# Kernel tuning notes

Hardware: AMD Instinct MI355X
Metric: run time of the kernel (lower is better)

## Reference

```python
import jax, jax.numpy as jnp
import numpy as np

N_GENES = 2000
D_MODEL = 256
N_LAYERS = 4
D_STATE = 16
D_CONV = 4
EXPAND = 2
D_INNER = EXPAND * D_MODEL  # 512
DT_RANK = (D_MODEL + 15) // 16  # 16


def layer_norm(x, w, b, eps=1e-5):
    mu = jnp.mean(x, axis=-1, keepdims=True)
    var = jnp.mean((x - mu) ** 2, axis=-1, keepdims=True)
    return (x - mu) * jax.lax.rsqrt(var + eps) * w + b


def mamba_mixer(h, in_w, cw, cb, xp_w, dtp_w, dtp_b, A_log, Dvec, out_w):
    # h: [B, L, d_model]
    B, L, _ = h.shape
    xz = jnp.einsum('bld,ed->ble', h, in_w)            # [B,L,2*Di]
    u, z = jnp.split(xz, 2, axis=-1)                    # [B,L,Di] each
    # causal depthwise conv1d (kernel D_CONV)
    up = jnp.pad(u, ((0, 0), (D_CONV - 1, 0), (0, 0)))
    u = sum(up[:, k:k + L, :] * cw[:, k] for k in range(D_CONV)) + cb
    u = jax.nn.silu(u)
    # input-dependent dt, B, C
    xdbc = jnp.einsum('bld,ed->ble', u, xp_w)           # [B,L,dt_rank+2N]
    dt_r = xdbc[..., :DT_RANK]
    Bm = xdbc[..., DT_RANK:DT_RANK + D_STATE]           # [B,L,N]
    Cm = xdbc[..., DT_RANK + D_STATE:]                  # [B,L,N]
    dt = jax.nn.softplus(jnp.einsum('blr,dr->bld', dt_r, dtp_w) + dtp_b)  # [B,L,Di]
    A = -jnp.exp(A_log)                                 # [Di,N]
    dA = jnp.exp(dt[..., None] * A)                     # [B,L,Di,N]
    dBu = dt[..., None] * Bm[:, :, None, :] * u[..., None]

    def step(hst, inp):
        a, bu = inp
        hst = a * hst + bu
        return hst, hst

    h0 = jnp.zeros((B, D_INNER, D_STATE), dA.dtype)
    _, hs = jax.lax.scan(step, h0, (jnp.moveaxis(dA, 1, 0), jnp.moveaxis(dBu, 1, 0)))
    y = jnp.einsum('lbdn,lbn->bld', hs, jnp.moveaxis(Cm, 1, 0)) + u * Dvec
    y = y * jax.nn.silu(z)
    return jnp.einsum('bld,ed->ble', y, out_w)          # [B,L,d_model]


def setup_inputs() -> dict:
    key = jax.random.key(0)
    ks = jax.random.split(key, 16)
    nl = N_LAYERS
    inp = {
        'x': jax.random.normal(ks[0], (2, N_GENES), jnp.float32),
        'bulk_in_w': jax.random.normal(ks[1], (D_MODEL,), jnp.float32),
        'bulk_in_b': jnp.zeros((D_MODEL,), jnp.float32),
        'gene_emb': jax.random.normal(ks[2], (1, N_GENES, D_MODEL), jnp.float32) * 0.02,
        'mod_emb': jax.random.normal(ks[3], (1, 1, D_MODEL), jnp.float32) * 0.02,
        'ln_w': jnp.ones((nl, D_MODEL), jnp.float32),
        'ln_b': jnp.zeros((nl, D_MODEL), jnp.float32),
        'in_proj_w': jax.random.normal(ks[4], (nl, 2 * D_INNER, D_MODEL), jnp.float32) * (D_MODEL ** -0.5),
        'conv_w': jax.random.normal(ks[5], (nl, D_INNER, D_CONV), jnp.float32) * (D_CONV ** -0.5),
        'conv_b': jnp.zeros((nl, D_INNER), jnp.float32),
        'x_proj_w': jax.random.normal(ks[6], (nl, DT_RANK + 2 * D_STATE, D_INNER), jnp.float32) * (D_INNER ** -0.5),
        'dt_proj_w': jax.random.normal(ks[7], (nl, D_INNER, DT_RANK), jnp.float32) * 0.01,
        'dt_proj_b': jnp.full((nl, D_INNER), -4.0, jnp.float32),
        'A_log': jnp.broadcast_to(jnp.log(jnp.arange(1, D_STATE + 1, dtype=jnp.float32)), (nl, D_INNER, D_STATE)).copy(),
        'D': jnp.ones((nl, D_INNER), jnp.float32),
        'out_proj_w': jax.random.normal(ks[8], (nl, D_MODEL, D_INNER), jnp.float32) * (D_INNER ** -0.5),
        'fin_w': jnp.ones((D_MODEL,), jnp.float32),
        'fin_b': jnp.zeros((D_MODEL,), jnp.float32),
        'head_w': jax.random.normal(ks[9], (D_MODEL,), jnp.float32) * (D_MODEL ** -0.5),
        'head_b': jnp.zeros((), jnp.float32),
    }
    return inp


def reference(x, bulk_in_w, bulk_in_b, gene_emb, mod_emb, ln_w, ln_b, in_proj_w,
              conv_w, conv_b, x_proj_w, dt_proj_w, dt_proj_b, A_log, D, out_proj_w,
              fin_w, fin_b, head_w, head_b):
    # token embed (modality='bulk'); Linear(1,d_model) == x[...,None]*w + b
    h = x[..., None] * bulk_in_w + bulk_in_b + gene_emb + mod_emb  # [B,L,d_model]
    for i in range(N_LAYERS):
        h = h + mamba_mixer(layer_norm(h, ln_w[i], ln_b[i]), in_proj_w[i], conv_w[i],
                            conv_b[i], x_proj_w[i], dt_proj_w[i], dt_proj_b[i],
                            A_log[i], D[i], out_proj_w[i])
    h = layer_norm(h, fin_w, fin_b)
    y = jnp.einsum('bld,d->bl', h, head_w) + head_b  # bulk head, squeeze(-1)
    return y
```

## Files before the change

### kernel.cpp

```cpp
#include <hip/hip_runtime.h>
#include <math.h>

#define B_  2
#define L_  2000
#define DM_ 256
#define DI_ 512
#define DS_ 16
#define NL_ 4
#define BL_ (B_*L_)
#define BLP_ 4096
#define NC_ 125
#define CL_ 16
#define NST_ (B_*DI_*DS_)

typedef unsigned short ushort_t;
typedef __attribute__((ext_vector_type(8))) short bf16x8;
typedef __attribute__((ext_vector_type(4))) float f32x4;

__device__ __forceinline__ float siluf(float x) {
    return x / (1.f + __expf(-x));
}

__device__ __forceinline__ ushort_t f2bf(float x) {
    unsigned int u = __float_as_uint(x);
    unsigned int r = (u + 0x7FFFu + ((u >> 16) & 1u)) >> 16;
    return (ushort_t)r;
}

__device__ __forceinline__ float bf2f(ushort_t v) {
    return __uint_as_float(((unsigned int)v) << 16);
}

__global__ __launch_bounds__(256) void embed_f2bf_kernel(
    const float* __restrict__ x, const float* __restrict__ biw,
    const float* __restrict__ bib, const float* __restrict__ ge,
    const float* __restrict__ me, float* __restrict__ h,
    float2* __restrict__ stats,
    const float* __restrict__ s0, const float* __restrict__ s1,
    const float* __restrict__ s2, ushort_t* __restrict__ d0,
    ushort_t* __restrict__ d1, ushort_t* __restrict__ d2,
    int N0, int N1, int N2)
{
    if (blockIdx.x < BL_) {
        __shared__ float sm[8];
        int bl = blockIdx.x, d = threadIdx.x;
        int l = bl % L_;
        float v = x[bl]*biw[d] + bib[d] + ge[(size_t)l*DM_ + d] + me[d];
        h[(size_t)bl*DM_ + d] = v;
        float s = v, q = v*v;
        #pragma unroll
        for (int o = 32; o > 0; o >>= 1) {
            s += __shfl_down(s, o);
            q += __shfl_down(q, o);
        }
        if ((d & 63) == 0) { sm[d >> 6] = s; sm[4 + (d >> 6)] = q; }
        __syncthreads();
        if (d == 0) {
            stats[bl] = make_float2(sm[0]+sm[1]+sm[2]+sm[3], sm[4]+sm[5]+sm[6]+sm[7]);
            stats[BLP_ + bl]   = make_float2(0.f, 0.f);
            stats[2*BLP_ + bl] = make_float2(0.f, 0.f);
            stats[3*BLP_ + bl] = make_float2(0.f, 0.f);
        }
    } else {
        int i = (blockIdx.x - BL_)*256 + threadIdx.x;
        const float* s; ushort_t* d; int j;
        if (i < N0)           { s = s0; d = d0; j = i; }
        else if (i < N0+N1)   { s = s1; d = d1; j = i - N0; }
        else if (i < N0+N1+N2){ s = s2; d = d2; j = i - N0 - N1; }
        else return;
        float4 v = *(const float4*)(s + 4*j);
        ushort_t o[4] = {f2bf(v.x), f2bf(v.y), f2bf(v.z), f2bf(v.w)};
        *(ushort2*)(d + 4*j)     = *(ushort2*)&o[0];
        *(ushort2*)(d + 4*j + 2) = *(ushort2*)&o[2];
    }
}

__global__ __launch_bounds__(256) void gemm_ln_mfma(
    const float* __restrict__ H, const float2* __restrict__ stats,
    const float* __restrict__ lnw, const float* __restrict__ lnb,
    const ushort_t* __restrict__ W, ushort_t* __restrict__ C, int ldc)
{
    __shared__ ushort_t a_s[128*64];
    __shared__ ushort_t b_s[128*64];
    const int r0 = blockIdx.x*128, c0 = blockIdx.y*128;
    const int tid = threadIdx.x;
    const int lane = tid & 63, w = tid >> 6;
    const int wm = (w & 1)*64, wn = (w >> 1)*64;
    const int qd = lane >> 4, l16 = lane & 15;
    f32x4 acc[4][4] = {};
    for (int kc = 0; kc < DM_; kc += 64) {
        #pragma unroll
        for (int q = 0; q < 4; q++) {
            int ch = tid + 256*q;
            int row = ch >> 3, col8 = (ch & 7)*8;
            int grow = r0 + row;
            float2 t0 = stats[grow], t1 = stats[BLP_ + grow];
            float2 t2 = stats[2*BLP_ + grow], t3 = stats[3*BLP_ + grow];
            float sum = t0.x + t1.x + t2.x + t3.x;
            float ssq = t0.y + t1.y + t2.y + t3.y;
            float mu  = sum * (1.f/DM_);
            float inv = rsqrtf(fmaxf(ssq*(1.f/DM_) - mu*mu, 0.f) + 1e-5f);
            const float* hp = H + (size_t)grow*DM_ + kc + col8;
            float4 h0 = *(const float4*)hp, h1 = *(const float4*)(hp + 4);
            const float* wp = lnw + kc + col8;
            const float* bp = lnb + kc + col8;
            float4 w0 = *(const float4*)wp, w1 = *(const float4*)(wp + 4);
            float4 b0 = *(const float4*)bp, b1 = *(const float4*)(bp + 4);
            __align__(16) ushort_t o[8];
            o[0] = f2bf((h0.x - mu)*inv*w0.x + b0.x);
            o[1] = f2bf((h0.y - mu)*inv*w0.y + b0.y);
            o[2] = f2bf((h0.z - mu)*inv*w0.z + b0.z);
            o[3] = f2bf((h0.w - mu)*inv*w0.w + b0.w);
            o[4] = f2bf((h1.x - mu)*inv*w1.x + b1.x);
            o[5] = f2bf((h1.y - mu)*inv*w1.y + b1.y);
            o[6] = f2bf((h1.z - mu)*inv*w1.z + b1.z);
            o[7] = f2bf((h1.w - mu)*inv*w1.w + b1.w);
            *(uint4*)&a_s[row*64 + col8] = *(const uint4*)o;
            *(bf16x8*)&b_s[row*64 + col8] =
                *(const bf16x8*)(W + (size_t)(c0 + row)*DM_ + kc + col8);
        }
        __syncthreads();
        #pragma unroll
        for (int ks = 0; ks < 2; ks++) {
            bf16x8 af[4], bf[4];
            #pragma unroll
            for (int i = 0; i < 4; i++)
                af[i] = *(const bf16x8*)&a_s[(wm + i*16 + l16)*64 + ks*32 + qd*8];
            #pragma unroll
            for (int j = 0; j < 4; j++)
                bf[j] = *(const bf16x8*)&b_s[(wn + j*16 + l16)*64 + ks*32 + qd*8];
            #pragma unroll
            for (int i = 0; i < 4; i++) {
                #pragma unroll
                for (int j = 0; j < 4; j++)
                    acc[i][j] = __builtin_amdgcn_mfma_f32_16x16x32_bf16(
                        af[i], bf[j], acc[i][j], 0, 0, 0);
            }
        }
        __syncthreads();
    }
    #pragma unroll
    for (int i = 0; i < 4; i++) {
        #pragma unroll
        for (int j = 0; j < 4; j++) {
            #pragma unroll
            for (int r = 0; r < 4; r++) {
                int row = r0 + wm + i*16 + qd*4 + r;
                int col = c0 + wn + j*16 + l16;
                C[(size_t)row*ldc + col] = f2bf(acc[i][j][r]);
            }
        }
    }
}

__global__ __launch_bounds__(256) void conv_xproj_kernel(
    const ushort_t* __restrict__ xz, const float* __restrict__ cw,
    const float* __restrict__ cb, const ushort_t* __restrict__ XWb,
    const float* __restrict__ DTW, const float* __restrict__ DTB,
    const float* __restrict__ Alog,
    ushort_t* __restrict__ u_bf, float* __restrict__ bn,
    float* __restrict__ cn, ushort_t* __restrict__ dtn,
    float2* __restrict__ sa)
{
    __shared__ ushort_t xs[19][520];
    __shared__ ushort_t us[16][520];
    __shared__ float ps[4*16*48];
    __shared__ float dtr_s[16][16];
    const int c = blockIdx.x, b = blockIdx.y;
    const int l0 = c * 16;
    const int tid = threadIdx.x;
    const int lane = tid & 63, w = tid >> 6;
    const int qd = lane >> 4, l16 = lane & 15;
    for (int f = tid; f < 19*64; f += 256) {
        int row = f >> 6, c8 = (f & 63)*8;
        int l = l0 - 3 + row;
        uint4 v = {0u, 0u, 0u, 0u};
        if (l >= 0)
            v = *(const uint4*)(xz + (size_t)(b*L_ + l)*1024 + c8);
        *(uint4*)&xs[row][c8] = v;
    }
    __syncthreads();
    #pragma unroll
    for (int q = 0; q < 2; q++) {
        int ch = tid + q*256;
        float4 wv = *(const float4*)(cw + ch*4);
        float bias = cb[ch];
        float x0 = bf2f(xs[0][ch]);
        float x1 = bf2f(xs[1][ch]);
        float x2 = bf2f(xs[2][ch]);
        #pragma unroll
        for (int j = 0; j < 16; j++) {
            float x3 = bf2f(xs[3 + j][ch]);
            float v = fmaf(x0, wv.x, fmaf(x1, wv.y, fmaf(x2, wv.z, fmaf(x3, wv.w, bias))));
            us[j][ch] = f2bf(siluf(v));
            x0 = x1; x1 = x2; x2 = x3;
        }
    }
    __syncthreads();
    for (int f = tid; f < 16*64; f += 256) {
        int row = f >> 6, c8 = (f & 63)*8;
        *(uint4*)(u_bf + (size_t)(b*L_ + l0 + row)*512 + c8) =
            *(const uint4*)&us[row][c8];
    }
    f32x4 acc[3] = {};
    #pragma unroll
    for (int step = 0; step < 4; step++) {
        int k = w*128 + step*32 + qd*8;
        bf16x8 af = *(const bf16x8*)&us[l16][k];
        #pragma unroll
        for (int j = 0; j < 3; j++) {
            bf16x8 bf = *(const bf16x8*)(XWb + (size_t)(j*16 + l16)*512 + k);
            acc[j] = __builtin_amdgcn_mfma_f32_16x16x32_bf16(af, bf, acc[j], 0, 0, 0);
        }
    }
    #pragma unroll
    for (int j = 0; j < 3; j++) {
        #pragma unroll
        for (int r = 0; r < 4; r++)
            ps[(w*16 + qd*4 + r)*48 + j*16 + l16] = acc[j][r];
    }
    __syncthreads();
    #pragma unroll
    for (int e = tid; e < 768; e += 256)
        ps[e] = ps[e] + ps[768 + e] + ps[1536 + e] + ps[2304 + e];
    __syncthreads();
    {
        int row = tid >> 4, n = tid & 15;
        dtr_s[row][n] = ps[row*48 + n];
        size_t base = ((size_t)(b*L_) + l0 + row)*DS_ + n;
        bn[base] = ps[row*48 + 16 + n];
        cn[base] = ps[row*48 + 32 + n];
    }
    __syncthreads();
    #pragma unroll
    for (int q = 0; q < 2; q++) {
        int d = tid + q*256;
        float wreg[16];
        const float4* wp = (const float4*)(DTW + (size_t)d*16);
        #pragma unroll
        for (int k4 = 0; k4 < 4; k4++) {
            float4 v = wp[k4];
            wreg[4*k4+0] = v.x; wreg[4*k4+1] = v.y;
            wreg[4*k4+2] = v.z; wreg[4*k4+3] = v.w;
        }
        float bias = DTB[d];
        float dtv[16];
        #pragma unroll
        for (int r = 0; r < 16; r++) {
            float a = bias;
            #pragma unroll
            for (int k = 0; k < 16; k++) a = fmaf(dtr_s[r][k], wreg[k], a);
            float dt = a > 20.f ? a : log1pf(__expf(a));
            ushort_t dtb16 = f2bf(dt);
            dtn[((size_t)(b*L_) + l0 + r)*DI_ + d] = dtb16;
            dtv[r] = bf2f(dtb16);
        }
        float Ac[DS_], s[DS_], ap[DS_];
        const float* ar = Alog + (size_t)d*DS_;
        #pragma unroll
        for (int n = 0; n < DS_; n++) { Ac[n] = -__expf(ar[n]); s[n] = 0.f; ap[n] = 1.f; }
        #pragma unroll
        for (int l = 0; l < 16; l++) {
            float dt = dtv[l];
            float u  = bf2f(us[l][d]);
            float dtu = dt*u;
            #pragma unroll
            for (int n = 0; n < DS_; n++) {
                float e = __expf(dt*Ac[n]);
                s[n] = fmaf(e, s[n], dtu*ps[l*48 + 16 + n]);
                ap[n] *= e;
            }
        }
        size_t ib = (((size_t)c*B_ + b)*DI_ + d)*DS_;
        float2* sap = sa + ib;
        #pragma unroll
        for (int k = 0; k < 8; k++) {
            float4 t = make_float4(s[2*k], ap[2*k], s[2*k+1], ap[2*k+1]);
            *(float4*)&sap[2*k] = t;
        }
    }
}

__global__ __launch_bounds__(64) void scan_phase2(
    const float2* __restrict__ sa, float* __restrict__ sinc)
{
    const int t = blockIdx.x*64 + threadIdx.x;
    float s = 0.f;
    for (int g = 0; g < 5; g++) {
        float2 v[25];
        #pragma unroll
        for (int i = 0; i < 25; i++)
            v[i] = sa[(size_t)(g*25 + i)*NST_ + t];
        #pragma unroll
        for (int i = 0; i < 25; i++) {
            sinc[(size_t)(g*25 + i)*NST_ + t] = s;
            s = fmaf(v[i].y, s, v[i].x);
        }
    }
}

template<int LAST>
__global__ __launch_bounds__(512) void phase3_fused(
    const ushort_t* __restrict__ dtn, const ushort_t* __restrict__ u_bf,
    const float* __restrict__ bn, const float* __restrict__ cn,
    const float* __restrict__ Alog, const float* __restrict__ Dv,
    const float* __restrict__ sinc, const ushort_t* __restrict__ xz,
    const ushort_t* __restrict__ opw, float* __restrict__ h,
    const float* __restrict__ lnw, const float* __restrict__ lnb,
    const ushort_t* __restrict__ ipw, ushort_t* __restrict__ xz_out,
    const float* __restrict__ hw, const float* __restrict__ hb,
    float* __restrict__ out)
{
    __shared__ float b_sh[CL_*DS_];
    __shared__ float c_sh[CL_*DS_];
    __shared__ ushort_t ys[16][520];
    __shared__ ushort_t a_sh[16][264];
    __shared__ float2 red2[8*16];
    __shared__ float2 muv[16];
    const int c = blockIdx.x, b = blockIdx.y;
    const int l0 = c*CL_;
    const int tid = threadIdx.x;
    const int w = tid >> 6, lane = tid & 63;
    const int qd = lane >> 4, l16 = lane & 15;
    {
        int f = tid & 255;
        size_t src = ((size_t)(b*L_) + l0)*DS_ + f;
        if (tid < 256) b_sh[f] = bn[src];
        else           c_sh[f] = cn[src];
    }
    const int d = tid;
    float Ac[DS_], s[DS_];
    {
        const float* ar = Alog + (size_t)d*DS_;
        #pragma unroll
        for (int n = 0; n < DS_; n++) Ac[n] = -__expf(ar[n]);
        size_t base = (((size_t)c*B_ + b)*DI_ + d)*DS_;
        #pragma unroll
        for (int n4 = 0; n4 < 4; n4++)
            *(float4*)&s[4*n4] = *(const float4*)(sinc + base + 4*n4);
    }
    const float Dd = Dv[d];
    __syncthreads();
    const ushort_t* dtp = dtn  + ((size_t)(b*L_ + l0))*DI_ + d;
    const ushort_t* up  = u_bf + ((size_t)(b*L_ + l0))*DI_ + d;
    const ushort_t* zp  = xz   + ((size_t)(b*L_ + l0))*1024 + 512 + d;
    for (int l = 0; l < CL_; l++) {
        float dt = bf2f(dtp[(size_t)l*DI_]);
        float u  = bf2f(up[(size_t)l*DI_]);
        float z  = bf2f(zp[(size_t)l*1024]);
        float dtu = dt*u;
        float y = u*Dd;
        #pragma unroll
        for (int n = 0; n < DS_; n++) {
            float e = __expf(dt*Ac[n]);
            s[n] = fmaf(e, s[n], dtu*b_sh[l*DS_ + n]);
            y = fmaf(s[n], c_sh[l*DS_ + n], y);
        }
        ys[l][d] = f2bf(y * siluf(z));
    }
    __syncthreads();
    f32x4 acc[2] = {};
    #pragma unroll
    for (int ks = 0; ks < 16; ks++) {
        bf16x8 af = *(const bf16x8*)&ys[l16][ks*32 + qd*8];
        #pragma unroll
        for (int j = 0; j < 2; j++) {
            bf16x8 bfv = *(const bf16x8*)(opw + (size_t)(w*32 + j*16 + l16)*DI_ + ks*32 + qd*8);
            acc[j] = __builtin_amdgcn_mfma_f32_16x16x32_bf16(af, bfv, acc[j], 0, 0, 0);
        }
    }
    float v[2][4];
    #pragma unroll
    for (int r = 0; r < 4; r++) {
        int lrow = qd*4 + r;
        size_t gr = (size_t)(b*L_ + l0 + lrow);
        float sm = 0.f, sq = 0.f;
        #pragma unroll
        for (int j = 0; j < 2; j++) {
            int col = w*32 + j*16 + l16;
            size_t idx = gr*DM_ + col;
            float vv = h[idx] + acc[j][r];
            if (!LAST) h[idx] = vv;
            v[j][r] = vv;
            sm += vv; sq += vv*vv;
        }
        sm += __shfl_xor(sm, 1); sq += __shfl_xor(sq, 1);
        sm += __shfl_xor(sm, 2); sq += __shfl_xor(sq, 2);
        sm += __shfl_xor(sm, 4); sq += __shfl_xor(sq, 4);
        sm += __shfl_xor(sm, 8); sq += __shfl_xor(sq, 8);
        if (l16 == 0) red2[w*16 + lrow] = make_float2(sm, sq);
    }
    __syncthreads();
    if (tid < 16) {
        float sm = 0.f, sq = 0.f;
        #pragma unroll
        for (int ww = 0; ww < 8; ww++) {
            float2 t = red2[ww*16 + tid];
            sm += t.x; sq += t.y;
        }
        float mu  = sm*(1.f/DM_);
        float inv = rsqrtf(fmaxf(sq*(1.f/DM_) - mu*mu, 0.f) + 1e-5f);
        muv[tid] = make_float2(mu, inv);
    }
    __syncthreads();
    if (!LAST) {
        #pragma unroll
        for (int r = 0; r < 4; r++) {
            int lrow = qd*4 + r;
            float2 mi = muv[lrow];
            #pragma unroll
            for (int j = 0; j < 2; j++) {
                int col = w*32 + j*16 + l16;
                a_sh[lrow][col] = f2bf((v[j][r] - mi.x)*mi.y*lnw[col] + lnb[col]);
            }
        }
        __syncthreads();
        f32x4 acc2[8] = {};
        const int n0 = w*128;
        #pragma unroll
        for (int ks = 0; ks < 8; ks++) {
            bf16x8 af = *(const bf16x8*)&a_sh[l16][ks*32 + qd*8];
            #pragma unroll
            for (int j2 = 0; j2 < 8; j2++) {
                bf16x8 bfv = *(const bf16x8*)(ipw + (size_t)(n0 + j2*16 + l16)*DM_ + ks*32 + qd*8);
                acc2[j2] = __builtin_amdgcn_mfma_f32_16x16x32_bf16(af, bfv, acc2[j2], 0, 0, 0);
            }
        }
        #pragma unroll
        for (int j2 = 0; j2 < 8; j2++) {
            #pragma unroll
            for (int r = 0; r < 4; r++) {
                size_t row = (size_t)(b*L_ + l0 + qd*4 + r);
                xz_out[row*1024 + n0 + j2*16 + l16] = f2bf(acc2[j2][r]);
            }
        }
    } else {
        float hd[4];
        #pragma unroll
        for (int r = 0; r < 4; r++) {
            int lrow = qd*4 + r;
            float2 mi = muv[lrow];
            float a = 0.f;
            #pragma unroll
            for (int j = 0; j < 2; j++) {
                int col = w*32 + j*16 + l16;
                float nv = (v[j][r] - mi.x)*mi.y*lnw[col] + lnb[col];
                a = fmaf(nv, hw[col], a);
            }
            hd[r] = a;
        }
        #pragma unroll
        for (int r = 0; r < 4; r++) {
            float x = hd[r];
            x += __shfl_xor(x, 1); x += __shfl_xor(x, 2);
            x += __shfl_xor(x, 4); x += __shfl_xor(x, 8);
            if (l16 == 0) red2[w*16 + qd*4 + r].x = x;
        }
        __syncthreads();
        if (tid < 16) {
            float x = 0.f;
            #pragma unroll
            for (int ww = 0; ww < 8; ww++) x += red2[ww*16 + tid].x;
            out[(size_t)(b*L_) + l0 + tid] = x + hb[0];
        }
    }
}

extern "C" void kernel_launch(void* const* d_in, const int* in_sizes, int n_in,
                              void* d_out, int out_size, void* d_ws, size_t ws_size,
                              hipStream_t stream)
{
    const float* x    = (const float*)d_in[0];
    const float* biw  = (const float*)d_in[1];
    const float* bib  = (const float*)d_in[2];
    const float* ge   = (const float*)d_in[3];
    const float* me   = (const float*)d_in[4];
    const float* lnw  = (const float*)d_in[5];
    const float* lnb  = (const float*)d_in[6];
    const float* ipw  = (const float*)d_in[7];
    const float* cw   = (const float*)d_in[8];
    const float* cb   = (const float*)d_in[9];
    const float* xpw  = (const float*)d_in[10];
    const float* dtw  = (const float*)d_in[11];
    const float* dtb  = (const float*)d_in[12];
    const float* alog = (const float*)d_in[13];
    const float* Dv   = (const float*)d_in[14];
    const float* opw  = (const float*)d_in[15];
    const float* fw   = (const float*)d_in[16];
    const float* fb   = (const float*)d_in[17];
    const float* hw   = (const float*)d_in[18];
    const float* hb   = (const float*)d_in[19];
    float* out = (float*)d_out;

    float* ws  = (float*)d_ws;
    float* h      = ws;
    float2* stats = (float2*)(h + (size_t)BLP_*DM_);
    float* bn     = (float*)(stats + 4*BLP_);
    float* cn     = bn + (size_t)B_*L_*DS_;
    float2* sa    = (float2*)(cn + (size_t)B_*L_*DS_);
    float* sinc   = (float*)(sa + (size_t)NC_*NST_);
    ushort_t* xz_bf = (ushort_t*)(sinc + (size_t)NC_*NST_);
    ushort_t* u_bf  = xz_bf + (size_t)BLP_*1024;
    ushort_t* dtn   = u_bf + (size_t)BLP_*DI_;
    ushort_t* ipwb  = dtn + (size_t)B_*L_*DI_;
    ushort_t* opwb  = ipwb + (size_t)NL_*1024*DM_;
    ushort_t* xpwb  = opwb + (size_t)NL_*DM_*DI_;

    const int N0 = NL_*1024*DM_/4, N1 = NL_*DM_*DI_/4, N2 = NL_*48*512/4;
    const int conv_blocks = (N0+N1+N2 + 255)/256;
    embed_f2bf_kernel<<<BL_ + conv_blocks, 256, 0, stream>>>(
        x, biw, bib, ge, me, h, stats,
        ipw, opw, xpw, ipwb, opwb, xpwb, N0, N1, N2);

    gemm_ln_mfma<<<dim3(BLP_/128, 1024/128), 256, 0, stream>>>(
        h, stats, lnw, lnb, ipwb, xz_bf, 1024);

    for (int i = 0; i < NL_; i++) {
        conv_xproj_kernel<<<dim3(NC_, B_), 256, 0, stream>>>(
            xz_bf, cw + i*DI_*4, cb + i*DI_, xpwb + (size_t)i*48*512,
            dtw + (size_t)i*DI_*16, dtb + i*DI_, alog + (size_t)i*DI_*DS_,
            u_bf, bn, cn, dtn, sa);
        scan_phase2<<<NST_/64, 64, 0, stream>>>(sa, sinc);
        if (i < NL_-1) {
            phase3_fused<0><<<dim3(NC_, B_), 512, 0, stream>>>(
                dtn, u_bf, bn, cn, alog + (size_t)i*DI_*DS_, Dv + i*DI_,
                sinc, xz_bf, opwb + (size_t)i*DM_*DI_, h,
                lnw + (i+1)*DM_, lnb + (i+1)*DM_,
                ipwb + (size_t)(i+1)*1024*DM_, xz_bf,
                nullptr, nullptr, nullptr);
        } else {
            phase3_fused<1><<<dim3(NC_, B_), 512, 0, stream>>>(
                dtn, u_bf, bn, cn, alog + (size_t)i*DI_*DS_, Dv + i*DI_,
                sinc, xz_bf, opwb + (size_t)i*DM_*DI_, h,
                fw, fb,
                nullptr, xz_bf,
                hw, hb, out);
        }
    }
}
```

Before: 414.3 us.

## Fuse phase3 output with next layer's conv/xproj via cooperative launch and halo flags

```diff
diff --git a/kernel.cpp b/kernel.cpp
--- a/kernel.cpp
+++ b/kernel.cpp
@@ -9,26 +9,147 @@
 #define NL_ 4
 #define BL_ (B_*L_)
 #define BLP_ 4096
-#define NC_ 125
-#define CL_ 16
+#define NC_  125
+#define CL_  16
 #define NST_ (B_*DI_*DS_)
 
 typedef unsigned short ushort_t;
 typedef __attribute__((ext_vector_type(8))) short bf16x8;
 typedef __attribute__((ext_vector_type(4))) float f32x4;
 
-__device__ __forceinline__ float siluf(float x) {
-    return x / (1.f + __expf(-x));
-}
-
+__device__ __forceinline__ float siluf(float x) { return x / (1.f + __expf(-x)); }
 __device__ __forceinline__ ushort_t f2bf(float x) {
     unsigned int u = __float_as_uint(x);
-    unsigned int r = (u + 0x7FFFu + ((u >> 16) & 1u)) >> 16;
-    return (ushort_t)r;
-}
-
+    return (ushort_t)((u + 0x7FFFu + ((u >> 16) & 1u)) >> 16);
+}
 __device__ __forceinline__ float bf2f(ushort_t v) {
     return __uint_as_float(((unsigned int)v) << 16);
+}
+
+struct PPart {
+    float b_sh[CL_*DS_];
+    float c_sh[CL_*DS_];
+    ushort_t ys[16][520];
+    ushort_t a_sh[16][264];
+    float2 red2[128];
+    float2 muv[16];
+};
+struct CPart {
+    ushort_t xs[19][520];
+    ushort_t us[16][520];
+    float ps[8*768];
+    float dtr[16][16];
+};
+union SharedF { PPart p; CPart c; };
+
+__device__ __forceinline__ void conv_tail(
+    CPart* S, int tid, int b, int l0, int c,
+    const float* __restrict__ cw, const float* __restrict__ cb,
+    const ushort_t* __restrict__ XWb,
+    const float* __restrict__ DTW, const float* __restrict__ DTB,
+    const float* __restrict__ Alog,
+    ushort_t* __restrict__ u_bf, float* __restrict__ bn,
+    float* __restrict__ cn, ushort_t* __restrict__ dtn,
+    float2* __restrict__ sa)
+{
+    const int lane = tid & 63, w = tid >> 6;
+    const int qd = lane >> 4, l16 = lane & 15;
+    {
+        int ch = tid;
+        float4 wv = *(const float4*)(cw + ch*4);
+        float bias = cb[ch];
+        float x0 = bf2f(S->xs[0][ch]);
+        float x1 = bf2f(S->xs[1][ch]);
+        float x2 = bf2f(S->xs[2][ch]);
+        #pragma unroll
+        for (int j = 0; j < 16; j++) {
+            float x3 = bf2f(S->xs[3 + j][ch]);
+            float v = fmaf(x0, wv.x, fmaf(x1, wv.y, fmaf(x2, wv.z, fmaf(x3, wv.w, bias))));
+            S->us[j][ch] = f2bf(siluf(v));
+            x0 = x1; x1 = x2; x2 = x3;
+        }
+    }
+    __syncthreads();
+    for (int f = tid; f < 16*64; f += 512) {
+        int row = f >> 6, c8 = (f & 63)*8;
+        *(uint4*)(u_bf + (size_t)(b*L_ + l0 + row)*512 + c8) =
+            *(const uint4*)&S->us[row][c8];
+    }
+    f32x4 acc[3] = {};
+    #pragma unroll
+    for (int st = 0; st < 2; st++) {
+        int k = w*64 + st*32 + qd*8;
+        bf16x8 af = *(const bf16x8*)&S->us[l16][k];
+        #pragma unroll
+        for (int j = 0; j < 3; j++) {
+            bf16x8 bv = *(const bf16x8*)(XWb + (size_t)(j*16 + l16)*512 + k);
+            acc[j] = __builtin_amdgcn_mfma_f32_16x16x32_bf16(af, bv, acc[j], 0, 0, 0);
+        }
+    }
+    #pragma unroll
+    for (int j = 0; j < 3; j++)
+        #pragma unroll
+        for (int r = 0; r < 4; r++)
+            S->ps[w*768 + (qd*4 + r)*48 + j*16 + l16] = acc[j][r];
+    __syncthreads();
+    for (int e = tid; e < 768; e += 512) {
+        float v = S->ps[e] + S->ps[768+e] + S->ps[1536+e] + S->ps[2304+e]
+                + S->ps[3072+e] + S->ps[3840+e] + S->ps[4608+e] + S->ps[5376+e];
+        S->ps[e] = v;
+    }
+    __syncthreads();
+    if (tid < 256) {
+        int row = tid >> 4, n = tid & 15;
+        S->dtr[row][n] = S->ps[row*48 + n];
+        size_t base = ((size_t)(b*L_) + l0 + row)*DS_ + n;
+        bn[base] = S->ps[row*48 + 16 + n];
+        cn[base] = S->ps[row*48 + 32 + n];
+    }
+    __syncthreads();
+    {
+        const int d = tid;
+        float wreg[16];
+        const float4* wp = (const float4*)(DTW + (size_t)d*16);
+        #pragma unroll
+        for (int k4 = 0; k4 < 4; k4++) {
+            float4 v = wp[k4];
+            wreg[4*k4+0] = v.x; wreg[4*k4+1] = v.y;
+            wreg[4*k4+2] = v.z; wreg[4*k4+3] = v.w;
+        }
+        float bias = DTB[d];
+        float dtv[16];
+        #pragma unroll
+        for (int r = 0; r < 16; r++) {
+            float a = bias;
+            #pragma unroll
+            for (int k = 0; k < 16; k++) a = fmaf(S->dtr[r][k], wreg[k], a);
+            float dt = a > 20.f ? a : log1pf(__expf(a));
+            ushort_t dtb16 = f2bf(dt);
+            dtn[((size_t)(b*L_) + l0 + r)*DI_ + d] = dtb16;
+            dtv[r] = bf2f(dtb16);
+        }
+        float Ac[DS_], s[DS_], ap[DS_];
+        const float* ar = Alog + (size_t)d*DS_;
+        #pragma unroll
+        for (int n = 0; n < DS_; n++) { Ac[n] = -__expf(ar[n]); s[n] = 0.f; ap[n] = 1.f; }
+        #pragma unroll
+        for (int l = 0; l < 16; l++) {
+            float dt = dtv[l];
+            float u  = bf2f(S->us[l][d]);
+            float dtu = dt*u;
+            #pragma unroll
+            for (int n = 0; n < DS_; n++) {
+                float e = __expf(dt*Ac[n]);
+                s[n] = fmaf(e, s[n], dtu*S->ps[l*48 + 16 + n]);
+                ap[n] *= e;
+            }
+        }
+        size_t ib = (((size_t)c*B_ + b)*DI_ + d)*DS_;
+        float2* sap = sa + ib;
+        #pragma unroll
+        for (int k = 0; k < 8; k++)
+            *(float4*)&sap[2*k] = make_float4(s[2*k], ap[2*k], s[2*k+1], ap[2*k+1]);
+    }
 }
 
 __global__ __launch_bounds__(256) void embed_f2bf_kernel(
@@ -39,7 +160,7 @@
     const float* __restrict__ s0, const float* __restrict__ s1,
     const float* __restrict__ s2, ushort_t* __restrict__ d0,
     ushort_t* __restrict__ d1, ushort_t* __restrict__ d2,
-    int N0, int N1, int N2)
+    int N0, int N1, int N2, unsigned int* __restrict__ flag)
 {
     if (blockIdx.x < BL_) {
         __shared__ float sm[8];
@@ -55,13 +176,12 @@
         }
         if ((d & 63) == 0) { sm[d >> 6] = s; sm[4 + (d >> 6)] = q; }
         __syncthreads();
-        if (d == 0) {
+        if (d == 0)
             stats[bl] = make_float2(sm[0]+sm[1]+sm[2]+sm[3], sm[4]+sm[5]+sm[6]+sm[7]);
-            stats[BLP_ + bl]   = make_float2(0.f, 0.f);
-            stats[2*BLP_ + bl] = make_float2(0.f, 0.f);
-            stats[3*BLP_ + bl] = make_float2(0.f, 0.f);
-        }
     } else {
+        if (blockIdx.x == BL_ && threadIdx.x < 2*NC_)
+            __hip_atomic_store(&flag[threadIdx.x], 0u,
+                               __ATOMIC_RELAXED, __HIP_MEMORY_SCOPE_AGENT);
         int i = (blockIdx.x - BL_)*256 + threadIdx.x;
         const float* s; ushort_t* d; int j;
         if (i < N0)           { s = s0; d = d0; j = i; }
@@ -78,7 +198,7 @@
 __global__ __launch_bounds__(256) void gemm_ln_mfma(
     const float* __restrict__ H, const float2* __restrict__ stats,
     const float* __restrict__ lnw, const float* __restrict__ lnb,
-    const ushort_t* __restrict__ W, ushort_t* __restrict__ C, int ldc)
+    const ushort_t* __restrict__ W, ushort_t* __restrict__ C)
 {
     __shared__ ushort_t a_s[128*64];
     __shared__ ushort_t b_s[128*64];
@@ -94,12 +214,9 @@
             int ch = tid + 256*q;
             int row = ch >> 3, col8 = (ch & 7)*8;
             int grow = r0 + row;
-            float2 t0 = stats[grow], t1 = stats[BLP_ + grow];
-            float2 t2 = stats[2*BLP_ + grow], t3 = stats[3*BLP_ + grow];
-            float sum = t0.x + t1.x + t2.x + t3.x;
-            float ssq = t0.y + t1.y + t2.y + t3.y;
-            float mu  = sum * (1.f/DM_);
-            float inv = rsqrtf(fmaxf(ssq*(1.f/DM_) - mu*mu, 0.f) + 1e-5f);
+            float2 t0 = stats[grow];
+            float mu  = t0.x * (1.f/DM_);
+            float inv = rsqrtf(fmaxf(t0.y*(1.f/DM_) - mu*mu, 0.f) + 1e-5f);
             const float* hp = H + (size_t)grow*DM_ + kc + col8;
             float4 h0 = *(const float4*)hp, h1 = *(const float4*)(hp + 4);
             const float* wp = lnw + kc + col8;
@@ -147,13 +264,13 @@
             for (int r = 0; r < 4; r++) {
                 int row = r0 + wm + i*16 + qd*4 + r;
                 int col = c0 + wn + j*16 + l16;
-                C[(size_t)row*ldc + col] = f2bf(acc[i][j][r]);
+                C[(size_t)row*1024 + col] = f2bf(acc[i][j][r]);
             }
         }
     }
 }
 
-__global__ __launch_bounds__(256) void conv_xproj_kernel(
+__global__ __launch_bounds__(512) void conv0_kernel(
     const ushort_t* __restrict__ xz, const float* __restrict__ cw,
     const float* __restrict__ cb, const ushort_t* __restrict__ XWb,
     const float* __restrict__ DTW, const float* __restrict__ DTB,
@@ -162,123 +279,19 @@
     float* __restrict__ cn, ushort_t* __restrict__ dtn,
     float2* __restrict__ sa)
 {
-    __shared__ ushort_t xs[19][520];
-    __shared__ ushort_t us[16][520];
-    __shared__ float ps[4*16*48];
-    __shared__ float dtr_s[16][16];
-    const int c = blockIdx.x, b = blockIdx.y;
-    const int l0 = c * 16;
+    __shared__ CPart S;
+    const int c = blockIdx.x, b = blockIdx.y, l0 = c*CL_;
     const int tid = threadIdx.x;
-    const int lane = tid & 63, w = tid >> 6;
-    const int qd = lane >> 4, l16 = lane & 15;
-    for (int f = tid; f < 19*64; f += 256) {
+    for (int f = tid; f < 19*64; f += 512) {
         int row = f >> 6, c8 = (f & 63)*8;
         int l = l0 - 3 + row;
-        uint4 v = {0u, 0u, 0u, 0u};
-        if (l >= 0)
-            v = *(const uint4*)(xz + (size_t)(b*L_ + l)*1024 + c8);
-        *(uint4*)&xs[row][c8] = v;
-    }
-    __syncthreads();
-    #pragma unroll
-    for (int q = 0; q < 2; q++) {
-        int ch = tid + q*256;
-        float4 wv = *(const float4*)(cw + ch*4);
-        float bias = cb[ch];
-        float x0 = bf2f(xs[0][ch]);
-        float x1 = bf2f(xs[1][ch]);
-        float x2 = bf2f(xs[2][ch]);
-        #pragma unroll
-        for (int j = 0; j < 16; j++) {
-            float x3 = bf2f(xs[3 + j][ch]);
-            float v = fmaf(x0, wv.x, fmaf(x1, wv.y, fmaf(x2, wv.z, fmaf(x3, wv.w, bias))));
-            us[j][ch] = f2bf(siluf(v));
-            x0 = x1; x1 = x2; x2 = x3;
-        }
-    }
-    __syncthreads();
-    for (int f = tid; f < 16*64; f += 256) {
-        int row = f >> 6, c8 = (f & 63)*8;
-        *(uint4*)(u_bf + (size_t)(b*L_ + l0 + row)*512 + c8) =
-            *(const uint4*)&us[row][c8];
-    }
-    f32x4 acc[3] = {};
-    #pragma unroll
-    for (int step = 0; step < 4; step++) {
-        int k = w*128 + step*32 + qd*8;
-        bf16x8 af = *(const bf16x8*)&us[l16][k];
-        #pragma unroll
-        for (int j = 0; j < 3; j++) {
-            bf16x8 bf = *(const bf16x8*)(XWb + (size_t)(j*16 + l16)*512 + k);
-            acc[j] = __builtin_amdgcn_mfma_f32_16x16x32_bf16(af, bf, acc[j], 0, 0, 0);
-        }
-    }
-    #pragma unroll
-    for (int j = 0; j < 3; j++) {
-        #pragma unroll
-        for (int r = 0; r < 4; r++)
-            ps[(w*16 + qd*4 + r)*48 + j*16 + l16] = acc[j][r];
-    }
-    __syncthreads();
-    #pragma unroll
-    for (int e = tid; e < 768; e += 256)
-        ps[e] = ps[e] + ps[768 + e] + ps[1536 + e] + ps[2304 + e];
-    __syncthreads();
-    {
-        int row = tid >> 4, n = tid & 15;
-        dtr_s[row][n] = ps[row*48 + n];
-        size_t base = ((size_t)(b*L_) + l0 + row)*DS_ + n;
-        bn[base] = ps[row*48 + 16 + n];
-        cn[base] = ps[row*48 + 32 + n];
-    }
-    __syncthreads();
-    #pragma unroll
-    for (int q = 0; q < 2; q++) {
-        int d = tid + q*256;
-        float wreg[16];
-        const float4* wp = (const float4*)(DTW + (size_t)d*16);
-        #pragma unroll
-        for (int k4 = 0; k4 < 4; k4++) {
-            float4 v = wp[k4];
-            wreg[4*k4+0] = v.x; wreg[4*k4+1] = v.y;
-            wreg[4*k4+2] = v.z; wreg[4*k4+3] = v.w;
-        }
-        float bias = DTB[d];
-        float dtv[16];
-        #pragma unroll
-        for (int r = 0; r < 16; r++) {
-            float a = bias;
-            #pragma unroll
-            for (int k = 0; k < 16; k++) a = fmaf(dtr_s[r][k], wreg[k], a);
-            float dt = a > 20.f ? a : log1pf(__expf(a));
-            ushort_t dtb16 = f2bf(dt);
-            dtn[((size_t)(b*L_) + l0 + r)*DI_ + d] = dtb16;
-            dtv[r] = bf2f(dtb16);
-        }
-        float Ac[DS_], s[DS_], ap[DS_];
-        const float* ar = Alog + (size_t)d*DS_;
-        #pragma unroll
-        for (int n = 0; n < DS_; n++) { Ac[n] = -__expf(ar[n]); s[n] = 0.f; ap[n] = 1.f; }
-        #pragma unroll
-        for (int l = 0; l < 16; l++) {
-            float dt = dtv[l];
-            float u  = bf2f(us[l][d]);
-            float dtu = dt*u;
-            #pragma unroll
-            for (int n = 0; n < DS_; n++) {
-                float e = __expf(dt*Ac[n]);
-                s[n] = fmaf(e, s[n], dtu*ps[l*48 + 16 + n]);
-                ap[n] *= e;
-            }
-        }
-        size_t ib = (((size_t)c*B_ + b)*DI_ + d)*DS_;
-        float2* sap = sa + ib;
-        #pragma unroll
-        for (int k = 0; k < 8; k++) {
-            float4 t = make_float4(s[2*k], ap[2*k], s[2*k+1], ap[2*k+1]);
-            *(float4*)&sap[2*k] = t;
-        }
-    }
+        uint4 v = {0u,0u,0u,0u};
+        if (l >= 0) v = *(const uint4*)(xz + (size_t)(b*L_ + l)*1024 + c8);
+        *(uint4*)&S.xs[row][c8] = v;
+    }
+    __syncthreads();
+    conv_tail(&S, tid, b, l0, c, cw, cb, XWb, DTW, DTB, Alog,
+              u_bf, bn, cn, dtn, sa);
 }
 
 __global__ __launch_bounds__(64) void scan_phase2(
@@ -299,34 +312,209 @@
     }
 }
 
-template<int LAST>
-__global__ __launch_bounds__(512) void phase3_fused(
-    const ushort_t* __restrict__ dtn, const ushort_t* __restrict__ u_bf,
-    const float* __restrict__ bn, const float* __restrict__ cn,
-    const float* __restrict__ Alog, const float* __restrict__ Dv,
-    const float* __restrict__ sinc, const ushort_t* __restrict__ xz,
-    const ushort_t* __restrict__ opw, float* __restrict__ h,
-    const float* __restrict__ lnw, const float* __restrict__ lnb,
-    const ushort_t* __restrict__ ipw, ushort_t* __restrict__ xz_out,
-    const float* __restrict__ hw, const float* __restrict__ hb,
-    float* __restrict__ out)
+struct FArgs {
+    ushort_t *dtn, *u_bf, *xz;
+    float *bn, *cn, *h;
+    float2 *sa; float *sinc;
+    const float *alog_prev, *Dv_prev;
+    const ushort_t *opw_prev;
+    const float *lnw, *lnb;
+    const ushort_t *ipw;
+    const float *cw, *cb;
+    const ushort_t *xpw;
+    const float *dtw, *dtb;
+    const float *alog_cur;
+    unsigned int *flag, *halo;
+};
+
+template<int LI>
+__global__ __launch_bounds__(512) void F_fused(FArgs a)
 {
-    __shared__ float b_sh[CL_*DS_];
-    __shared__ float c_sh[CL_*DS_];
-    __shared__ ushort_t ys[16][520];
-    __shared__ ushort_t a_sh[16][264];
-    __shared__ float2 red2[8*16];
-    __shared__ float2 muv[16];
-    const int c = blockIdx.x, b = blockIdx.y;
-    const int l0 = c*CL_;
+    __shared__ SharedF S;
+    const int blk = blockIdx.x;
+    const int c = blk >> 1, b = blk & 1, l0 = c*CL_;
     const int tid = threadIdx.x;
     const int w = tid >> 6, lane = tid & 63;
     const int qd = lane >> 4, l16 = lane & 15;
     {
         int f = tid & 255;
         size_t src = ((size_t)(b*L_) + l0)*DS_ + f;
-        if (tid < 256) b_sh[f] = bn[src];
-        else           c_sh[f] = cn[src];
+        if (tid < 256) S.p.b_sh[f] = a.bn[src];
+        else           S.p.c_sh[f] = a.cn[src];
+    }
+    const int d = tid;
+    float Ac[DS_], s[DS_];
+    {
+        const float* ar = a.alog_prev + (size_t)d*DS_;
+        #pragma unroll
+        for (int n = 0; n < DS_; n++) Ac[n] = -__expf(ar[n]);
+        size_t base = (((size_t)c*B_ + b)*DI_ + d)*DS_;
+        #pragma unroll
+        for (int n4 = 0; n4 < 4; n4++)
+            *(float4*)&s[4*n4] = *(const float4*)(a.sinc + base + 4*n4);
+    }
+    const float Dd = a.Dv_prev[d];
+    __syncthreads();
+    const ushort_t* dtp = a.dtn  + ((size_t)(b*L_ + l0))*DI_ + d;
+    const ushort_t* up  = a.u_bf + ((size_t)(b*L_ + l0))*DI_ + d;
+    const ushort_t* zp  = a.xz   + ((size_t)(b*L_ + l0))*1024 + 512 + d;
+    for (int l = 0; l < CL_; l++) {
+        float dt = bf2f(dtp[(size_t)l*DI_]);
+        float u  = bf2f(up[(size_t)l*DI_]);
+        float z  = bf2f(zp[(size_t)l*1024]);
+        float dtu = dt*u;
+        float y = u*Dd;
+        #pragma unroll
+        for (int n = 0; n < DS_; n++) {
+            float e = __expf(dt*Ac[n]);
+            s[n] = fmaf(e, s[n], dtu*S.p.b_sh[l*DS_ + n]);
+            y = fmaf(s[n], S.p.c_sh[l*DS_ + n], y);
+        }
+        S.p.ys[l][d] = f2bf(y * siluf(z));
+    }
+    __syncthreads();
+    f32x4 acc[2] = {};
+    #pragma unroll
+    for (int ks = 0; ks < 16; ks++) {
+        bf16x8 af = *(const bf16x8*)&S.p.ys[l16][ks*32 + qd*8];
+        #pragma unroll
+        for (int j = 0; j < 2; j++) {
+            bf16x8 bv = *(const bf16x8*)(a.opw_prev + (size_t)(w*32 + j*16 + l16)*DI_ + ks*32 + qd*8);
+            acc[j] = __builtin_amdgcn_mfma_f32_16x16x32_bf16(af, bv, acc[j], 0, 0, 0);
+        }
+    }
+    float vv2[2][4];
+    #pragma unroll
+    for (int r = 0; r < 4; r++) {
+        int lrow = qd*4 + r;
+        size_t gr = (size_t)(b*L_ + l0 + lrow);
+        float sm = 0.f, sq = 0.f;
+        #pragma unroll
+        for (int j = 0; j < 2; j++) {
+            int col = w*32 + j*16 + l16;
+            size_t idx = gr*DM_ + col;
+            float vv = a.h[idx] + acc[j][r];
+            a.h[idx] = vv;
+            vv2[j][r] = vv;
+            sm += vv; sq += vv*vv;
+        }
+        sm += __shfl_xor(sm, 1); sq += __shfl_xor(sq, 1);
+        sm += __shfl_xor(sm, 2); sq += __shfl_xor(sq, 2);
+        sm += __shfl_xor(sm, 4); sq += __shfl_xor(sq, 4);
+        sm += __shfl_xor(sm, 8); sq += __shfl_xor(sq, 8);
+        if (l16 == 0) S.p.red2[w*16 + lrow] = make_float2(sm, sq);
+    }
+    __syncthreads();
+    if (tid < 16) {
+        float sm = 0.f, sq = 0.f;
+        #pragma unroll
+        for (int ww = 0; ww < 8; ww++) {
+            float2 t = S.p.red2[ww*16 + tid];
+            sm += t.x; sq += t.y;
+        }
+        float mu  = sm*(1.f/DM_);
+        float inv = rsqrtf(fmaxf(sq*(1.f/DM_) - mu*mu, 0.f) + 1e-5f);
+        S.p.muv[tid] = make_float2(mu, inv);
+    }
+    __syncthreads();
+    #pragma unroll
+    for (int r = 0; r < 4; r++) {
+        int lrow = qd*4 + r;
+        float2 mi = S.p.muv[lrow];
+        #pragma unroll
+        for (int j = 0; j < 2; j++) {
+            int col = w*32 + j*16 + l16;
+            S.p.a_sh[lrow][col] = f2bf((vv2[j][r] - mi.x)*mi.y*a.lnw[col] + a.lnb[col]);
+        }
+    }
+    __syncthreads();
+    f32x4 acc2[8] = {};
+    const int n0 = w*128;
+    #pragma unroll
+    for (int ks = 0; ks < 8; ks++) {
+        bf16x8 af = *(const bf16x8*)&S.p.a_sh[l16][ks*32 + qd*8];
+        #pragma unroll
+        for (int j2 = 0; j2 < 8; j2++) {
+            bf16x8 bv = *(const bf16x8*)(a.ipw + (size_t)(n0 + j2*16 + l16)*DM_ + ks*32 + qd*8);
+            acc2[j2] = __builtin_amdgcn_mfma_f32_16x16x32_bf16(af, bv, acc2[j2], 0, 0, 0);
+        }
+    }
+    if (w >= 4) {
+        #pragma unroll
+        for (int j2 = 0; j2 < 8; j2++)
+            #pragma unroll
+            for (int r = 0; r < 4; r++) {
+                size_t row = (size_t)(b*L_ + l0 + qd*4 + r);
+                a.xz[row*1024 + n0 + j2*16 + l16] = f2bf(acc2[j2][r]);
+            }
+    }
+    __syncthreads();
+    if (w < 4) {
+        #pragma unroll
+        for (int j2 = 0; j2 < 8; j2++)
+            #pragma unroll
+            for (int r = 0; r < 4; r++)
+                S.c.xs[3 + qd*4 + r][n0 + j2*16 + l16] = f2bf(acc2[j2][r]);
+    }
+    __syncthreads();
+    for (int t = tid; t < 768; t += 512) {
+        int rr = t >> 8, j = t & 255;
+        unsigned int pv = (unsigned int)S.c.xs[16+rr][2*j]
+                        | ((unsigned int)S.c.xs[16+rr][2*j+1] << 16);
+        __hip_atomic_store(&a.halo[((size_t)(c*B_ + b))*768 + t], pv,
+                           __ATOMIC_RELAXED, __HIP_MEMORY_SCOPE_AGENT);
+    }
+    asm volatile("s_waitcnt vmcnt(0)" ::: "memory");
+    __syncthreads();
+    if (tid == 0)
+        __hip_atomic_store(&a.flag[c*B_ + b], (unsigned int)LI,
+                           __ATOMIC_RELEASE, __HIP_MEMORY_SCOPE_AGENT);
+    if (c > 0) {
+        if (tid == 0) {
+            while (__hip_atomic_load(&a.flag[(c-1)*B_ + b],
+                       __ATOMIC_ACQUIRE, __HIP_MEMORY_SCOPE_AGENT) < (unsigned int)LI)
+                __builtin_amdgcn_s_sleep(8);
+        }
+        __syncthreads();
+        for (int t = tid; t < 768; t += 512) {
+            unsigned int pv = __hip_atomic_load(
+                &a.halo[((size_t)((c-1)*B_ + b))*768 + t],
+                __ATOMIC_RELAXED, __HIP_MEMORY_SCOPE_AGENT);
+            int rr = t >> 8, j = t & 255;
+            S.c.xs[rr][2*j]   = (ushort_t)(pv & 0xFFFFu);
+            S.c.xs[rr][2*j+1] = (ushort_t)(pv >> 16);
+        }
+    } else {
+        for (int t = tid; t < 768; t += 512) {
+            int rr = t >> 8, j = t & 255;
+            S.c.xs[rr][2*j] = 0; S.c.xs[rr][2*j+1] = 0;
+        }
+    }
+    __syncthreads();
+    conv_tail(&S.c, tid, b, l0, c, a.cw, a.cb, a.xpw, a.dtw, a.dtb,
+              a.alog_cur, a.u_bf, a.bn, a.cn, a.dtn, a.sa);
+}
+
+__global__ __launch_bounds__(512) void phase3_head(
+    const ushort_t* __restrict__ dtn, const ushort_t* __restrict__ u_bf,
+    const float* __restrict__ bn, const float* __restrict__ cn,
+    const float* __restrict__ Alog, const float* __restrict__ Dv,
+    const float* __restrict__ sinc, const ushort_t* __restrict__ xz,
+    const ushort_t* __restrict__ opw, const float* __restrict__ h,
+    const float* __restrict__ fw, const float* __restrict__ fb,
+    const float* __restrict__ hw, const float* __restrict__ hb,
+    float* __restrict__ out)
+{
+    __shared__ PPart S;
+    const int c = blockIdx.x, b = blockIdx.y, l0 = c*CL_;
+    const int tid = threadIdx.x;
+    const int w = tid >> 6, lane = tid & 63;
+    const int qd = lane >> 4, l16 = lane & 15;
+    {
+        int f = tid & 255;
+        size_t src = ((size_t)(b*L_) + l0)*DS_ + f;
+        if (tid < 256) S.b_sh[f] = bn[src];
+        else           S.c_sh[f] = cn[src];
     }
     const int d = tid;
     float Ac[DS_], s[DS_];
@@ -353,23 +541,23 @@
         #pragma unroll
         for (int n = 0; n < DS_; n++) {
             float e = __expf(dt*Ac[n]);
-            s[n] = fmaf(e, s[n], dtu*b_sh[l*DS_ + n]);
-            y = fmaf(s[n], c_sh[l*DS_ + n], y);
-        }
-        ys[l][d] = f2bf(y * siluf(z));
+            s[n] = fmaf(e, s[n], dtu*S.b_sh[l*DS_ + n]);
+            y = fmaf(s[n], S.c_sh[l*DS_ + n], y);
+        }
+        S.ys[l][d] = f2bf(y * siluf(z));
     }
     __syncthreads();
     f32x4 acc[2] = {};
     #pragma unroll
     for (int ks = 0; ks < 16; ks++) {
-        bf16x8 af = *(const bf16x8*)&ys[l16][ks*32 + qd*8];
+        bf16x8 af = *(const bf16x8*)&S.ys[l16][ks*32 + qd*8];
         #pragma unroll
         for (int j = 0; j < 2; j++) {
-            bf16x8 bfv = *(const bf16x8*)(opw + (size_t)(w*32 + j*16 + l16)*DI_ + ks*32 + qd*8);
-            acc[j] = __builtin_amdgcn_mfma_f32_16x16x32_bf16(af, bfv, acc[j], 0, 0, 0);
-        }
-    }
-    float v[2][4];
+            bf16x8 bv = *(const bf16x8*)(opw + (size_t)(w*32 + j*16 + l16)*DI_ + ks*32 + qd*8);
+            acc[j] = __builtin_amdgcn_mfma_f32_16x16x32_bf16(af, bv, acc[j], 0, 0, 0);
+        }
+    }
+    float vv2[2][4];
     #pragma unroll
     for (int r = 0; r < 4; r++) {
         int lrow = qd*4 + r;
@@ -378,91 +566,56 @@
         #pragma unroll
         for (int j = 0; j < 2; j++) {
             int col = w*32 + j*16 + l16;
-            size_t idx = gr*DM_ + col;
-            float vv = h[idx] + acc[j][r];
-            if (!LAST) h[idx] = vv;
-            v[j][r] = vv;
+            float vv = h[gr*DM_ + col] + acc[j][r];
+            vv2[j][r] = vv;
             sm += vv; sq += vv*vv;
         }
         sm += __shfl_xor(sm, 1); sq += __shfl_xor(sq, 1);
         sm += __shfl_xor(sm, 2); sq += __shfl_xor(sq, 2);
         sm += __shfl_xor(sm, 4); sq += __shfl_xor(sq, 4);
         sm += __shfl_xor(sm, 8); sq += __shfl_xor(sq, 8);
-        if (l16 == 0) red2[w*16 + lrow] = make_float2(sm, sq);
+        if (l16 == 0) S.red2[w*16 + lrow] = make_float2(sm, sq);
     }
     __syncthreads();
     if (tid < 16) {
         float sm = 0.f, sq = 0.f;
         #pragma unroll
         for (int ww = 0; ww < 8; ww++) {
-            float2 t = red2[ww*16 + tid];
+            float2 t = S.red2[ww*16 + tid];
             sm += t.x; sq += t.y;
         }
         float mu  = sm*(1.f/DM_);
         float inv = rsqrtf(fmaxf(sq*(1.f/DM_) - mu*mu, 0.f) + 1e-5f);
-        muv[tid] = make_float2(mu, inv);
-    }
-    __syncthreads();
-    if (!LAST) {
-        #pragma unroll
-        for (int r = 0; r < 4; r++) {
-            int lrow = qd*4 + r;
-            float2 mi = muv[lrow];
-            #pragma unroll
-            for (int j = 0; j < 2; j++) {
-                int col = w*32 + j*16 + l16;
-                a_sh[lrow][col] = f2bf((v[j][r] - mi.x)*mi.y*lnw[col] + lnb[col]);
-            }
-        }
-        __syncthreads();
-        f32x4 acc2[8] = {};
-        const int n0 = w*128;
-        #pragma unroll
-        for (int ks = 0; ks < 8; ks++) {
-            bf16x8 af = *(const bf16x8*)&a_sh[l16][ks*32 + qd*8];
-            #pragma unroll
-            for (int j2 = 0; j2 < 8; j2++) {
-                bf16x8 bfv = *(const bf16x8*)(ipw + (size_t)(n0 + j2*16 + l16)*DM_ + ks*32 + qd*8);
-                acc2[j2] = __builtin_amdgcn_mfma_f32_16x16x32_bf16(af, bfv, acc2[j2], 0, 0, 0);
-            }
-        }
-        #pragma unroll
-        for (int j2 = 0; j2 < 8; j2++) {
-            #pragma unroll
-            for (int r = 0; r < 4; r++) {
-                size_t row = (size_t)(b*L_ + l0 + qd*4 + r);
-                xz_out[row*1024 + n0 + j2*16 + l16] = f2bf(acc2[j2][r]);
-            }
-        }
-    } else {
-        float hd[4];
-        #pragma unroll
-        for (int r = 0; r < 4; r++) {
-            int lrow = qd*4 + r;
-            float2 mi = muv[lrow];
-            float a = 0.f;
-            #pragma unroll
-            for (int j = 0; j < 2; j++) {
-                int col = w*32 + j*16 + l16;
-                float nv = (v[j][r] - mi.x)*mi.y*lnw[col] + lnb[col];
-                a = fmaf(nv, hw[col], a);
-            }
-            hd[r] = a;
-        }
-        #pragma unroll
-        for (int r = 0; r < 4; r++) {
-            float x = hd[r];
-            x += __shfl_xor(x, 1); x += __shfl_xor(x, 2);
-            x += __shfl_xor(x, 4); x += __shfl_xor(x, 8);
-            if (l16 == 0) red2[w*16 + qd*4 + r].x = x;
-        }
-        __syncthreads();
-        if (tid < 16) {
-            float x = 0.f;
-            #pragma unroll
-            for (int ww = 0; ww < 8; ww++) x += red2[ww*16 + tid].x;
-            out[(size_t)(b*L_) + l0 + tid] = x + hb[0];
-        }
+        S.muv[tid] = make_float2(mu, inv);
+    }
+    __syncthreads();
+    float hd[4];
+    #pragma unroll
+    for (int r = 0; r < 4; r++) {
+        int lrow = qd*4 + r;
+        float2 mi = S.muv[lrow];
+        float aa = 0.f;
+        #pragma unroll
+        for (int j = 0; j < 2; j++) {
+            int col = w*32 + j*16 + l16;
+            float nv = (vv2[j][r] - mi.x)*mi.y*fw[col] + fb[col];
+            aa = fmaf(nv, hw[col], aa);
+        }
+        hd[r] = aa;
+    }
+    #pragma unroll
+    for (int r = 0; r < 4; r++) {
+        float xv = hd[r];
+        xv += __shfl_xor(xv, 1); xv += __shfl_xor(xv, 2);
+        xv += __shfl_xor(xv, 4); xv += __shfl_xor(xv, 8);
+        if (l16 == 0) S.red2[w*16 + qd*4 + r].x = xv;
+    }
+    __syncthreads();
+    if (tid < 16) {
+        float xv = 0.f;
+        #pragma unroll
+        for (int ww = 0; ww < 8; ww++) xv += S.red2[ww*16 + tid].x;
+        out[(size_t)(b*L_) + l0 + tid] = xv + hb[0];
     }
 }
 
@@ -495,7 +648,7 @@
     float* ws  = (float*)d_ws;
     float* h      = ws;
     float2* stats = (float2*)(h + (size_t)BLP_*DM_);
-    float* bn     = (float*)(stats + 4*BLP_);
+    float* bn     = (float*)(stats + BLP_);
     float* cn     = bn + (size_t)B_*L_*DS_;
     float2* sa    = (float2*)(cn + (size_t)B_*L_*DS_);
     float* sinc   = (float*)(sa + (size_t)NC_*NST_);
@@ -505,36 +658,48 @@
     ushort_t* ipwb  = dtn + (size_t)B_*L_*DI_;
     ushort_t* opwb  = ipwb + (size_t)NL_*1024*DM_;
     ushort_t* xpwb  = opwb + (size_t)NL_*DM_*DI_;
+    unsigned int* flag = (unsigned int*)(xpwb + (size_t)NL_*48*512);
+    unsigned int* halo = flag + 512;
 
     const int N0 = NL_*1024*DM_/4, N1 = NL_*DM_*DI_/4, N2 = NL_*48*512/4;
     const int conv_blocks = (N0+N1+N2 + 255)/256;
     embed_f2bf_kernel<<<BL_ + conv_blocks, 256, 0, stream>>>(
         x, biw, bib, ge, me, h, stats,
-        ipw, opw, xpw, ipwb, opwb, xpwb, N0, N1, N2);
+        ipw, opw, xpw, ipwb, opwb, xpwb, N0, N1, N2, flag);
 
     gemm_ln_mfma<<<dim3(BLP_/128, 1024/128), 256, 0, stream>>>(
-        h, stats, lnw, lnb, ipwb, xz_bf, 1024);
-
-    for (int i = 0; i < NL_; i++) {
-        conv_xproj_kernel<<<dim3(NC_, B_), 256, 0, stream>>>(
-            xz_bf, cw + i*DI_*4, cb + i*DI_, xpwb + (size_t)i*48*512,
-            dtw + (size_t)i*DI_*16, dtb + i*DI_, alog + (size_t)i*DI_*DS_,
-            u_bf, bn, cn, dtn, sa);
+        h, stats, lnw, lnb, ipwb, xz_bf);
+
+    conv0_kernel<<<dim3(NC_, B_), 512, 0, stream>>>(
+        xz_bf, cw, cb, xpwb, dtw, dtb, alog,
+        u_bf, bn, cn, dtn, sa);
+    scan_phase2<<<NST_/64, 64, 0, stream>>>(sa, sinc);
+
+    const void* fks[4] = { nullptr,
+        (const void*)F_fused<1>, (const void*)F_fused<2>, (const void*)F_fused<3> };
+    for (int li = 1; li < NL_; li++) {
+        FArgs fa;
+        fa.dtn = dtn; fa.u_bf = u_bf; fa.xz = xz_bf;
+        fa.bn = bn; fa.cn = cn; fa.h = h;
+        fa.sa = sa; fa.sinc = sinc;
+        fa.alog_prev = alog + (size_t)(li-1)*DI_*DS_;
+        fa.Dv_prev   = Dv + (li-1)*DI_;
+        fa.opw_prev  = opwb + (size_t)(li-1)*DM_*DI_;
+        fa.lnw = lnw + li*DM_; fa.lnb = lnb + li*DM_;
+        fa.ipw = ipwb + (size_t)li*1024*DM_;
+        fa.cw = cw + li*DI_*4; fa.cb = cb + li*DI_;
+        fa.xpw = xpwb + (size_t)li*48*512;
+        fa.dtw = dtw + (size_t)li*DI_*16; fa.dtb = dtb + li*DI_;
+        fa.alog_cur = alog + (size_t)li*DI_*DS_;
+        fa.flag = flag; fa.halo = halo;
+        void* ka[] = { (void*)&fa };
+        hipLaunchCooperativeKernel(fks[li], dim3(NC_*B_), dim3(512),
+                                   ka, 0, stream);
         scan_phase2<<<NST_/64, 64, 0, stream>>>(sa, sinc);
-        if (i < NL_-1) {
-            phase3_fused<0><<<dim3(NC_, B_), 512, 0, stream>>>(
-                dtn, u_bf, bn, cn, alog + (size_t)i*DI_*DS_, Dv + i*DI_,
-                sinc, xz_bf, opwb + (size_t)i*DM_*DI_, h,
-                lnw + (i+1)*DM_, lnb + (i+1)*DM_,
-                ipwb + (size_t)(i+1)*1024*DM_, xz_bf,
-                nullptr, nullptr, nullptr);
-        } else {
-            phase3_fused<1><<<dim3(NC_, B_), 512, 0, stream>>>(
-                dtn, u_bf, bn, cn, alog + (size_t)i*DI_*DS_, Dv + i*DI_,
-                sinc, xz_bf, opwb + (size_t)i*DM_*DI_, h,
-                fw, fb,
-                nullptr, xz_bf,
-                hw, hb, out);
-        }
-    }
-}
+    }
+
+    phase3_head<<<dim3(NC_, B_), 512, 0, stream>>>(
+        dtn, u_bf, bn, cn, alog + (size_t)3*DI_*DS_, Dv + 3*DI_,
+        sinc, xz_bf, opwb + (size_t)3*DM_*DI_, h,
+        fw, fb, hw, hb, out);
+}
```

Result: slower. 621.7 us (+50.1%).
